# Kernel tuning notes

Hardware: AMD Instinct MI355X
Metric: run time of the kernel (lower is better)

The kernel has to match this reference:

```python
import jax, jax.numpy as jnp
import numpy as np
import math

# ---- HashGridEncoder constants (from init_kwargs) ----
L = 16            # levels
LOG2T = 19
T = 1 << LOG2T    # hash table size per level
F = 2             # features per entry
N_MIN = 16
N_MAX = 2048
N_PTS = 524288    # number of query points
BB_MIN = np.zeros(3, np.float32)
BB_MAX = np.ones(3, np.float32)
B = math.exp((math.log(N_MAX) - math.log(N_MIN)) / (L - 1))
RES = np.array([math.floor(N_MIN * B ** i) for i in range(L)], dtype=np.float32)  # per-level grid resolution
VERTS = np.array([[0,0,0],[0,0,1],[0,1,0],[0,1,1],[1,0,0],[1,0,1],[1,1,0],[1,1,1]], dtype=np.int32)  # 8 cube corners
PI = np.array([1, 2654435761, 805459861], dtype=np.uint32)  # spatial hash primes
MASK = np.uint32((1 << 19) - 1)  # hard-coded mask from source


def setup_inputs() -> dict:
    key = jax.random.key(0)
    k1, k2 = jax.random.split(key)
    xyz = jax.random.uniform(k1, (N_PTS, 3), dtype=jnp.float32)  # points inside bbox [0,1]^3
    # nn.init.uniform_(weight, -1e-4, 1e-4)
    tables = jax.random.uniform(k2, (L, T, F), minval=-1e-4, maxval=1e-4, dtype=jnp.float32)
    return {"xyz": xyz, "tables": tables}


def reference(xyz, tables):
    # cell size per level: (bb_max - bb_min) / resolution  -> [L,3]
    cell = (BB_MAX - BB_MIN)[None, :] / RES[:, None]
    # normalized grid coords for all levels at once: [L,N,3]
    u = (xyz[None, :, :] - BB_MIN) / cell[:, None, :]
    mi = jnp.floor(u).astype(jnp.int32)            # min corner index [L,N,3]
    d = u - mi.astype(jnp.float32)                 # trilinear fracs == (xyz - min_vertex)/cell, [L,N,3]
    # 8 corner integer coords: [L,N,8,3]; uint32 wrapping matches int64-mul + low-19-bit mask
    corners = (mi[:, :, None, :] + VERTS[None, None]).astype(jnp.uint32)
    h = (corners[..., 0] * PI[0]) ^ (corners[..., 1] * PI[1]) ^ (corners[..., 2] * PI[2])
    h = (h & MASK).astype(jnp.int32)               # hash indices [L,N,8], all < T
    # gather all levels in one flat lookup
    flat = tables.reshape(L * T, F)
    idx = h + (jnp.arange(L, dtype=jnp.int32) * T)[:, None, None]
    emb = flat[idx]                                # [L,N,8,F]
    # trilinear weights: prod over axes of d (corner bit 1) or 1-d (corner bit 0) -> [L,N,8]
    w = jnp.prod(jnp.where(VERTS[None, None].astype(bool), d[:, :, None, :], 1.0 - d[:, :, None, :]), axis=-1)
    c = jnp.einsum('lnv,lnvf->lnf', w, emb)        # interpolated features [L,N,F]
    # torch.cat(embedded, dim=-1): level-major concat -> [N, L*F]
    return jnp.moveaxis(c, 0, 1).reshape(xyz.shape[0], L * F)
```

## Files before the change

### kernel.cpp

```cpp
#include <hip/hip_runtime.h>
#include <cmath>

#define NLEVELS 16
#define HMASK   0x7FFFFu
#define NPTS    524288
#define NBUCKET 32768

typedef float v4f __attribute__((ext_vector_type(4)));
typedef float v2f __attribute__((ext_vector_type(2)));

struct LevelParams {
    float cell[NLEVELS];
};

__device__ __forceinline__ unsigned spread5(unsigned v) {
    return (v & 1u) | ((v & 2u) << 2) | ((v & 4u) << 4) |
           ((v & 8u) << 6) | ((v & 16u) << 8);
}

__device__ __forceinline__ unsigned morton_key(float x, float y, float z) {
    unsigned bx = min(31u, (unsigned)(x * 32.0f));
    unsigned by = min(31u, (unsigned)(y * 32.0f));
    unsigned bz = min(31u, (unsigned)(z * 32.0f));
    return spread5(bx) | (spread5(by) << 1) | (spread5(bz) << 2);
}

__device__ __forceinline__ void ngp_hash(
    float x, float y, float z, float cell, unsigned* __restrict__ h,
    float& dx, float& dy, float& dz)
{
    const float ux = x / cell;
    const float uy = y / cell;
    const float uz = z / cell;
    const float fx = floorf(ux);
    const float fy = floorf(uy);
    const float fz = floorf(uz);
    dx = ux - fx;
    dy = uy - fy;
    dz = uz - fz;

    const unsigned ix = (unsigned)(int)fx;
    const unsigned iy = (unsigned)(int)fy;
    const unsigned iz = (unsigned)(int)fz;

    const unsigned hx0 = ix;
    const unsigned hx1 = ix + 1u;
    const unsigned hy0 = iy * 2654435761u;
    const unsigned hy1 = (iy + 1u) * 2654435761u;
    const unsigned hz0 = iz * 805459861u;
    const unsigned hz1 = (iz + 1u) * 805459861u;

    h[0] = (hx0 ^ hy0 ^ hz0) & HMASK;
    h[1] = (hx0 ^ hy0 ^ hz1) & HMASK;
    h[2] = (hx0 ^ hy1 ^ hz0) & HMASK;
    h[3] = (hx0 ^ hy1 ^ hz1) & HMASK;
    h[4] = (hx1 ^ hy0 ^ hz0) & HMASK;
    h[5] = (hx1 ^ hy0 ^ hz1) & HMASK;
    h[6] = (hx1 ^ hy1 ^ hz0) & HMASK;
    h[7] = (hx1 ^ hy1 ^ hz1) & HMASK;
}

__device__ __forceinline__ void ngp_weights(
    float dx, float dy, float dz, float* __restrict__ w)
{
    const float wx0 = 1.0f - dx;
    const float wy0 = 1.0f - dy;
    const float wz0 = 1.0f - dz;
    const float p00 = wx0 * wy0;
    const float p01 = wx0 * dy;
    const float p10 = dx * wy0;
    const float p11 = dx * dy;
    w[0] = p00 * wz0;
    w[1] = p00 * dz;
    w[2] = p01 * wz0;
    w[3] = p01 * dz;
    w[4] = p10 * wz0;
    w[5] = p10 * dz;
    w[6] = p11 * wz0;
    w[7] = p11 * dz;
}

__device__ __forceinline__ v2f ngp_combine(
    const float* __restrict__ w, const v2f* __restrict__ e)
{
    float c0 = w[0] * e[0].x;
    float c1 = w[0] * e[0].y;
    #pragma unroll
    for (int c = 1; c < 8; ++c) {
        c0 += w[c] * e[c].x;
        c1 += w[c] * e[c].y;
    }
    v2f r = { c0, c1 };
    return r;
}

__global__ __launch_bounds__(256) void bucket_count(
    const float* __restrict__ xyz, unsigned* __restrict__ counts)
{
    const int n = blockIdx.x * 256 + threadIdx.x;
    const float x = xyz[3 * n + 0];
    const float y = xyz[3 * n + 1];
    const float z = xyz[3 * n + 2];
    atomicAdd(&counts[morton_key(x, y, z)], 1u);
}

__global__ __launch_bounds__(1024) void bucket_scan(
    const unsigned* __restrict__ counts, unsigned* __restrict__ cursor)
{
    __shared__ unsigned c[NBUCKET];
    __shared__ unsigned psum[1024];
    const unsigned t = threadIdx.x;

    #pragma unroll
    for (int i = 0; i < 32; ++i) {
        const unsigned idx = (unsigned)i * 1024u + t;
        c[idx ^ ((idx >> 5) & 31u)] = counts[idx];
    }
    __syncthreads();

    unsigned s = 0;
    #pragma unroll
    for (int i = 0; i < 32; ++i) {
        const unsigned idx = t * 32u + (unsigned)i;
        s += c[idx ^ ((idx >> 5) & 31u)];
    }
    psum[t] = s;
    __syncthreads();

    for (unsigned off = 1; off < 1024; off <<= 1) {
        unsigned v = 0;
        if (t >= off) v = psum[t - off];
        __syncthreads();
        if (t >= off) psum[t] += v;
        __syncthreads();
    }

    unsigned excl = psum[t] - s;
    #pragma unroll
    for (int i = 0; i < 32; ++i) {
        const unsigned idx = t * 32u + (unsigned)i;
        const unsigned sw  = idx ^ ((idx >> 5) & 31u);
        const unsigned v = c[sw];
        c[sw] = excl;
        excl += v;
    }
    __syncthreads();

    #pragma unroll
    for (int i = 0; i < 32; ++i) {
        const unsigned idx = (unsigned)i * 1024u + t;
        cursor[idx] = c[idx ^ ((idx >> 5) & 31u)];
    }
}

__global__ __launch_bounds__(256) void bucket_scatter(
    const float* __restrict__ xyz, unsigned* __restrict__ cursor,
    v4f* __restrict__ pts)
{
    const int n = blockIdx.x * 256 + threadIdx.x;
    const float x = xyz[3 * n + 0];
    const float y = xyz[3 * n + 1];
    const float z = xyz[3 * n + 2];
    const unsigned key = morton_key(x, y, z);
    const unsigned p = atomicAdd(&cursor[key], 1u);
    v4f v = { x, y, z, __uint_as_float((unsigned)n) };
    pts[p] = v;
}

__global__ __launch_bounds__(256) void ngp_phase1(
    const v4f* __restrict__ pts,
    const float* __restrict__ tables,
    v2f* __restrict__ ws,
    LevelParams lp)
{
    const unsigned b = blockIdx.x;
    const int level = (int)(b >> 11);
    const int chunk = (int)(b & 2047u);
    const int p = chunk * 256 + threadIdx.x;

    const v4f q = pts[p];

    const float cell = lp.cell[level];
    const v2f* __restrict__ tab = (const v2f*)tables + ((size_t)level << 19);

    unsigned h[8];
    float dx, dy, dz;
    ngp_hash(q.x, q.y, q.z, cell, h, dx, dy, dz);

    v2f e[8];
    if (level >= 7) {
        v2f e0, e1, e2, e3, e4, e5, e6, e7;
        const v2f* a0 = tab + h[0];
        const v2f* a1 = tab + h[1];
        const v2f* a2 = tab + h[2];
        const v2f* a3 = tab + h[3];
        const v2f* a4 = tab + h[4];
        const v2f* a5 = tab + h[5];
        const v2f* a6 = tab + h[6];
        const v2f* a7 = tab + h[7];
        asm volatile(
            "global_load_dwordx2 %0, %8, off sc0\n\t"
            "global_load_dwordx2 %1, %9, off sc0\n\t"
            "global_load_dwordx2 %2, %10, off sc0\n\t"
            "global_load_dwordx2 %3, %11, off sc0\n\t"
            "global_load_dwordx2 %4, %12, off sc0\n\t"
            "global_load_dwordx2 %5, %13, off sc0\n\t"
            "global_load_dwordx2 %6, %14, off sc0\n\t"
            "global_load_dwordx2 %7, %15, off sc0\n\t"
            "s_waitcnt vmcnt(0)"
            : "=&v"(e0), "=&v"(e1), "=&v"(e2), "=&v"(e3),
              "=&v"(e4), "=&v"(e5), "=&v"(e6), "=&v"(e7)
            : "v"(a0), "v"(a1), "v"(a2), "v"(a3),
              "v"(a4), "v"(a5), "v"(a6), "v"(a7));
        e[0] = e0; e[1] = e1; e[2] = e2; e[3] = e3;
        e[4] = e4; e[5] = e5; e[6] = e6; e[7] = e7;
    } else {
        #pragma unroll
        for (int c = 0; c < 8; ++c) e[c] = tab[h[c]];
    }

    float w[8];
    ngp_weights(dx, dy, dz, w);

    const v2f r = ngp_combine(w, e);

    __builtin_nontemporal_store(r, &ws[(size_t)level * NPTS + p]);
}

#define P2S 257

__global__ __launch_bounds__(256) void ngp_phase2(
    const v2f* __restrict__ ws,
    const v4f* __restrict__ pts,
    float* __restrict__ out)
{
    __shared__ v2f lds[NLEVELS * P2S];
    __shared__ unsigned nperm[256];
    const unsigned base = blockIdx.x * 256;
    const unsigned t = threadIdx.x;

    nperm[t] = __float_as_uint(pts[base + t].w);
    #pragma unroll
    for (int l = 0; l < NLEVELS; ++l)
        lds[l * P2S + t] =
            __builtin_nontemporal_load(&ws[(size_t)l * NPTS + base + t]);

    __syncthreads();

    #pragma unroll
    for (int it = 0; it < 8; ++it) {
        const unsigned j = it * 256 + t;
        const unsigned pl = j >> 3;
        const unsigned k = j & 7u;
        const v2f a = lds[(2u * k)      * P2S + pl];
        const v2f b = lds[(2u * k + 1u) * P2S + pl];
        v4f v = { a.x, a.y, b.x, b.y };
        __builtin_nontemporal_store(
            v, (v4f*)(out + (size_t)nperm[pl] * 32 + k * 4));
    }
}

__global__ __launch_bounds__(256) void ngp_encode(
    const float* __restrict__ xyz,
    const float* __restrict__ tables,
    float* __restrict__ out,
    LevelParams lp)
{
    const int n = blockIdx.x * 256 + threadIdx.x;
    const float x = xyz[3 * n + 0];
    const float y = xyz[3 * n + 1];
    const float z = xyz[3 * n + 2];

    float acc[2 * NLEVELS];
    const v2f* __restrict__ tab_base = (const v2f*)tables;

    #pragma unroll
    for (int l = 0; l < NLEVELS; ++l) {
        unsigned h[8];
        float dx, dy, dz;
        ngp_hash(x, y, z, lp.cell[l], h, dx, dy, dz);
        const v2f* __restrict__ tab = tab_base + ((size_t)l << 19);
        v2f e[8];
        #pragma unroll
        for (int c = 0; c < 8; ++c) e[c] = tab[h[c]];
        float w[8];
        ngp_weights(dx, dy, dz, w);
        const v2f r = ngp_combine(w, e);
        acc[2 * l + 0] = r.x;
        acc[2 * l + 1] = r.y;
    }

    v4f* o4 = (v4f*)(out + (size_t)n * 32);
    #pragma unroll
    for (int j = 0; j < 8; ++j) {
        v4f v = { acc[4 * j + 0], acc[4 * j + 1],
                  acc[4 * j + 2], acc[4 * j + 3] };
        o4[j] = v;
    }
}

extern "C" void kernel_launch(void* const* d_in, const int* in_sizes, int n_in,
                              void* d_out, int out_size, void* d_ws, size_t ws_size,
                              hipStream_t stream) {
    const float* xyz    = (const float*)d_in[0];
    const float* tables = (const float*)d_in[1];
    float* out          = (float*)d_out;

    LevelParams lp;
    const double B = std::exp((std::log(2048.0) - std::log(16.0)) / 15.0);
    for (int i = 0; i < NLEVELS; ++i) {
        const double r = std::floor(16.0 * std::pow(B, (double)i));
        lp.cell[i] = 1.0f / (float)r;
    }

    const size_t off_feat   = 0;
    const size_t off_pts    = off_feat + (size_t)NLEVELS * NPTS * sizeof(v2f);
    const size_t off_counts = off_pts + (size_t)NPTS * sizeof(v4f);
    const size_t off_cursor = off_counts + (size_t)NBUCKET * sizeof(unsigned);
    const size_t ws_needed  = off_cursor + (size_t)NBUCKET * sizeof(unsigned);

    if (ws_size >= ws_needed) {
        char* wsb = (char*)d_ws;
        v2f*      ws_feat = (v2f*)(wsb + off_feat);
        v4f*      pts     = (v4f*)(wsb + off_pts);
        unsigned* counts  = (unsigned*)(wsb + off_counts);
        unsigned* cursor  = (unsigned*)(wsb + off_cursor);

        hipMemsetAsync(counts, 0, NBUCKET * sizeof(unsigned), stream);
        hipLaunchKernelGGL(bucket_count, dim3(NPTS / 256), dim3(256), 0, stream,
                           xyz, counts);
        hipLaunchKernelGGL(bucket_scan, dim3(1), dim3(1024), 0, stream,
                           counts, cursor);
        hipLaunchKernelGGL(bucket_scatter, dim3(NPTS / 256), dim3(256), 0, stream,
                           xyz, cursor, pts);
        hipLaunchKernelGGL(ngp_phase1, dim3(NLEVELS * (NPTS / 256)), dim3(256), 0, stream,
                           pts, tables, ws_feat, lp);
        hipLaunchKernelGGL(ngp_phase2, dim3(NPTS / 256), dim3(256), 0, stream,
                           ws_feat, pts, out);
    } else {
        hipLaunchKernelGGL(ngp_encode, dim3(NPTS / 256), dim3(256), 0, stream,
                           xyz, tables, out, lp);
    }
}
```

Before: 351.1 us.

## Process two points per thread in phase1 and use wave-shuffle scan

Phase1 now handles two points per thread. It issues 16 table gathers before waiting, and computes the first point's result while the second point's loads are still in flight (vmcnt(8)). This raises memory-level parallelism per wave. The inline-asm gather path now covers levels from 5 instead of 7. The bucket scan replaces the 1024-wide LDS Hillis-Steele loop, which had many barriers, with a wave-level shuffle scan plus a 16-entry wave-sum pass. More registers per thread may lower occupancy, and the grid is halved.

Result: no change. 351.1 us (+0.0%).

```diff
diff --git a/kernel.cpp b/kernel.cpp
--- a/kernel.cpp
+++ b/kernel.cpp
@@ -108,8 +108,10 @@
     const unsigned* __restrict__ counts, unsigned* __restrict__ cursor)
 {
     __shared__ unsigned c[NBUCKET];
-    __shared__ unsigned psum[1024];
+    __shared__ unsigned wsum[16];
     const unsigned t = threadIdx.x;
+    const unsigned lane = t & 63u;
+    const unsigned wid = t >> 6;
 
     #pragma unroll
     for (int i = 0; i < 32; ++i) {
@@ -124,25 +126,29 @@
         const unsigned idx = t * 32u + (unsigned)i;
         s += c[idx ^ ((idx >> 5) & 31u)];
     }
-    psum[t] = s;
+
+    unsigned v = s;
+    #pragma unroll
+    for (unsigned off = 1; off < 64; off <<= 1) {
+        const unsigned u = __shfl_up(v, off);
+        if (lane >= off) v += u;
+    }
+    if (lane == 63u) wsum[wid] = v;
     __syncthreads();
 
-    for (unsigned off = 1; off < 1024; off <<= 1) {
-        unsigned v = 0;
-        if (t >= off) v = psum[t - off];
-        __syncthreads();
-        if (t >= off) psum[t] += v;
-        __syncthreads();
-    }
-
-    unsigned excl = psum[t] - s;
+    unsigned woff = 0;
+    #pragma unroll
+    for (unsigned w = 0; w < 16; ++w)
+        woff += (w < wid) ? wsum[w] : 0u;
+
+    unsigned excl = woff + (v - s);
     #pragma unroll
     for (int i = 0; i < 32; ++i) {
         const unsigned idx = t * 32u + (unsigned)i;
         const unsigned sw  = idx ^ ((idx >> 5) & 31u);
-        const unsigned v = c[sw];
+        const unsigned tmp = c[sw];
         c[sw] = excl;
-        excl += v;
+        excl += tmp;
     }
     __syncthreads();
 
@@ -174,30 +180,26 @@
     LevelParams lp)
 {
     const unsigned b = blockIdx.x;
-    const int level = (int)(b >> 11);
-    const int chunk = (int)(b & 2047u);
-    const int p = chunk * 256 + threadIdx.x;
-
-    const v4f q = pts[p];
+    const int level = (int)(b >> 10);
+    const int chunk = (int)(b & 1023u);
+    const int p0 = chunk * 512 + threadIdx.x;
+    const int p1 = p0 + 256;
+
+    const v4f qa = pts[p0];
+    const v4f qb = pts[p1];
 
     const float cell = lp.cell[level];
     const v2f* __restrict__ tab = (const v2f*)tables + ((size_t)level << 19);
 
-    unsigned h[8];
-    float dx, dy, dz;
-    ngp_hash(q.x, q.y, q.z, cell, h, dx, dy, dz);
-
-    v2f e[8];
-    if (level >= 7) {
-        v2f e0, e1, e2, e3, e4, e5, e6, e7;
-        const v2f* a0 = tab + h[0];
-        const v2f* a1 = tab + h[1];
-        const v2f* a2 = tab + h[2];
-        const v2f* a3 = tab + h[3];
-        const v2f* a4 = tab + h[4];
-        const v2f* a5 = tab + h[5];
-        const v2f* a6 = tab + h[6];
-        const v2f* a7 = tab + h[7];
+    unsigned ha[8], hb[8];
+    float dxa, dya, dza, dxb, dyb, dzb;
+    ngp_hash(qa.x, qa.y, qa.z, cell, ha, dxa, dya, dza);
+    ngp_hash(qb.x, qb.y, qb.z, cell, hb, dxb, dyb, dzb);
+
+    v2f ea[8], eb[8];
+    if (level >= 5) {
+        v2f a0, a1, a2, a3, a4, a5, a6, a7;
+        v2f b0, b1, b2, b3, b4, b5, b6, b7;
         asm volatile(
             "global_load_dwordx2 %0, %8, off sc0\n\t"
             "global_load_dwordx2 %1, %9, off sc0\n\t"
@@ -206,25 +208,63 @@
             "global_load_dwordx2 %4, %12, off sc0\n\t"
             "global_load_dwordx2 %5, %13, off sc0\n\t"
             "global_load_dwordx2 %6, %14, off sc0\n\t"
-            "global_load_dwordx2 %7, %15, off sc0\n\t"
+            "global_load_dwordx2 %7, %15, off sc0"
+            : "=&v"(a0), "=&v"(a1), "=&v"(a2), "=&v"(a3),
+              "=&v"(a4), "=&v"(a5), "=&v"(a6), "=&v"(a7)
+            : "v"(tab + ha[0]), "v"(tab + ha[1]), "v"(tab + ha[2]), "v"(tab + ha[3]),
+              "v"(tab + ha[4]), "v"(tab + ha[5]), "v"(tab + ha[6]), "v"(tab + ha[7]));
+        asm volatile(
+            "global_load_dwordx2 %0, %8, off sc0\n\t"
+            "global_load_dwordx2 %1, %9, off sc0\n\t"
+            "global_load_dwordx2 %2, %10, off sc0\n\t"
+            "global_load_dwordx2 %3, %11, off sc0\n\t"
+            "global_load_dwordx2 %4, %12, off sc0\n\t"
+            "global_load_dwordx2 %5, %13, off sc0\n\t"
+            "global_load_dwordx2 %6, %14, off sc0\n\t"
+            "global_load_dwordx2 %7, %15, off sc0"
+            : "=&v"(b0), "=&v"(b1), "=&v"(b2), "=&v"(b3),
+              "=&v"(b4), "=&v"(b5), "=&v"(b6), "=&v"(b7)
+            : "v"(tab + hb[0]), "v"(tab + hb[1]), "v"(tab + hb[2]), "v"(tab + hb[3]),
+              "v"(tab + hb[4]), "v"(tab + hb[5]), "v"(tab + hb[6]), "v"(tab + hb[7]));
+        asm volatile(
+            "s_waitcnt vmcnt(8)"
+            : "+v"(a0), "+v"(a1), "+v"(a2), "+v"(a3),
+              "+v"(a4), "+v"(a5), "+v"(a6), "+v"(a7));
+        ea[0] = a0; ea[1] = a1; ea[2] = a2; ea[3] = a3;
+        ea[4] = a4; ea[5] = a5; ea[6] = a6; ea[7] = a7;
+
+        float wa[8];
+        ngp_weights(dxa, dya, dza, wa);
+        const v2f ra = ngp_combine(wa, ea);
+
+        asm volatile(
             "s_waitcnt vmcnt(0)"
-            : "=&v"(e0), "=&v"(e1), "=&v"(e2), "=&v"(e3),
-              "=&v"(e4), "=&v"(e5), "=&v"(e6), "=&v"(e7)
-            : "v"(a0), "v"(a1), "v"(a2), "v"(a3),
-              "v"(a4), "v"(a5), "v"(a6), "v"(a7));
-        e[0] = e0; e[1] = e1; e[2] = e2; e[3] = e3;
-        e[4] = e4; e[5] = e5; e[6] = e6; e[7] = e7;
+            : "+v"(b0), "+v"(b1), "+v"(b2), "+v"(b3),
+              "+v"(b4), "+v"(b5), "+v"(b6), "+v"(b7));
+        eb[0] = b0; eb[1] = b1; eb[2] = b2; eb[3] = b3;
+        eb[4] = b4; eb[5] = b5; eb[6] = b6; eb[7] = b7;
+
+        float wb[8];
+        ngp_weights(dxb, dyb, dzb, wb);
+        const v2f rb = ngp_combine(wb, eb);
+
+        __builtin_nontemporal_store(ra, &ws[(size_t)level * NPTS + p0]);
+        __builtin_nontemporal_store(rb, &ws[(size_t)level * NPTS + p1]);
     } else {
         #pragma unroll
-        for (int c = 0; c < 8; ++c) e[c] = tab[h[c]];
-    }
-
-    float w[8];
-    ngp_weights(dx, dy, dz, w);
-
-    const v2f r = ngp_combine(w, e);
-
-    __builtin_nontemporal_store(r, &ws[(size_t)level * NPTS + p]);
+        for (int c = 0; c < 8; ++c) ea[c] = tab[ha[c]];
+        #pragma unroll
+        for (int c = 0; c < 8; ++c) eb[c] = tab[hb[c]];
+
+        float wa[8], wb[8];
+        ngp_weights(dxa, dya, dza, wa);
+        ngp_weights(dxb, dyb, dzb, wb);
+        const v2f ra = ngp_combine(wa, ea);
+        const v2f rb = ngp_combine(wb, eb);
+
+        __builtin_nontemporal_store(ra, &ws[(size_t)level * NPTS + p0]);
+        __builtin_nontemporal_store(rb, &ws[(size_t)level * NPTS + p1]);
+    }
 }
 
 #define P2S 257
@@ -333,7 +373,7 @@
                            counts, cursor);
         hipLaunchKernelGGL(bucket_scatter, dim3(NPTS / 256), dim3(256), 0, stream,
                            xyz, cursor, pts);
-        hipLaunchKernelGGL(ngp_phase1, dim3(NLEVELS * (NPTS / 256)), dim3(256), 0, stream,
+        hipLaunchKernelGGL(ngp_phase1, dim3(NLEVELS * (NPTS / 512)), dim3(256), 0, stream,
                            pts, tables, ws_feat, lp);
         hipLaunchKernelGGL(ngp_phase2, dim3(NPTS / 256), dim3(256), 0, stream,
                            ws_feat, pts, out);
```

## Fuse bucket sort into cooperative kernel and pair adjacent hash entries into 16-byte loads

Applied to the files above, without the earlier changes.

Replaces the memset, count, scan and scatter launches with one cooperative kernel that uses grid-wide syncs, removing several launches and the serial single-block scan. In phase1, levels from 5 upward use four dwordx4 loads when the x-corner index is even, because the x0 and x1 corner hashes then differ only in the low bit and share one aligned 16-byte slot. This cuts gather instructions for about half the points. The fallback bucket_scan also switches to a wave-shuffle scan. Risks include cooperative launch overhead and the cost of the grid syncs.

After: 793.0 us. 126% more time.

```diff
diff --git a/kernel.cpp b/kernel.cpp
--- a/kernel.cpp
+++ b/kernel.cpp
@@ -1,10 +1,14 @@
 #include <hip/hip_runtime.h>
+#include <hip/hip_cooperative_groups.h>
 #include <cmath>
+
+namespace cg = cooperative_groups;
 
 #define NLEVELS 16
 #define HMASK   0x7FFFFu
 #define NPTS    524288
 #define NBUCKET 32768
+#define SORTBLK 1024
 
 typedef float v4f __attribute__((ext_vector_type(4)));
 typedef float v2f __attribute__((ext_vector_type(2)));
@@ -27,7 +31,7 @@
 
 __device__ __forceinline__ void ngp_hash(
     float x, float y, float z, float cell, unsigned* __restrict__ h,
-    float& dx, float& dy, float& dz)
+    float& dx, float& dy, float& dz, unsigned& ix_out)
 {
     const float ux = x / cell;
     const float uy = y / cell;
@@ -42,6 +46,7 @@
     const unsigned ix = (unsigned)(int)fx;
     const unsigned iy = (unsigned)(int)fy;
     const unsigned iz = (unsigned)(int)fz;
+    ix_out = ix;
 
     const unsigned hx0 = ix;
     const unsigned hx1 = ix + 1u;
@@ -94,6 +99,95 @@
     return r;
 }
 
+__global__ __launch_bounds__(256, 4) void sort_coop(
+    const float* __restrict__ xyz,
+    v4f* __restrict__ pts,
+    unsigned* __restrict__ counts,
+    unsigned* __restrict__ cursor,
+    unsigned* __restrict__ bsum)
+{
+    cg::grid_group grid = cg::this_grid();
+    const unsigned b = blockIdx.x;
+    const unsigned t = threadIdx.x;
+    const unsigned lane = t & 63u;
+    const unsigned gtid = b * 256u + t;
+
+    if (gtid < NBUCKET) counts[gtid] = 0u;
+    grid.sync();
+
+    #pragma unroll
+    for (int k = 0; k < 2; ++k) {
+        const unsigned n = gtid + (unsigned)k * (NPTS / 2);
+        const float x = xyz[3 * n + 0];
+        const float y = xyz[3 * n + 1];
+        const float z = xyz[3 * n + 2];
+        atomicAdd(&counts[morton_key(x, y, z)], 1u);
+    }
+    grid.sync();
+
+    if (t < 64u) {
+        unsigned v = (t < 32u) ? counts[b * 32u + t] : 0u;
+        #pragma unroll
+        for (unsigned off = 1; off < 64; off <<= 1)
+            v += __shfl_xor(v, off);
+        if (t == 0u) bsum[b] = v;
+    }
+    grid.sync();
+
+    if (b == 0u) {
+        __shared__ unsigned wtot[4];
+        const unsigned wid = t >> 6;
+        const unsigned base = t * 4u;
+        const unsigned v0 = bsum[base + 0];
+        const unsigned v1 = bsum[base + 1];
+        const unsigned v2 = bsum[base + 2];
+        const unsigned v3 = bsum[base + 3];
+        const unsigned s = v0 + v1 + v2 + v3;
+        unsigned incl = s;
+        #pragma unroll
+        for (unsigned off = 1; off < 64; off <<= 1) {
+            const unsigned u = __shfl_up(incl, off);
+            if (lane >= off) incl += u;
+        }
+        if (lane == 63u) wtot[wid] = incl;
+        __syncthreads();
+        unsigned woff = 0;
+        #pragma unroll
+        for (unsigned w = 0; w < 4; ++w)
+            woff += (w < wid) ? wtot[w] : 0u;
+        const unsigned excl = woff + incl - s;
+        bsum[base + 0] = excl;
+        bsum[base + 1] = excl + v0;
+        bsum[base + 2] = excl + v0 + v1;
+        bsum[base + 3] = excl + v0 + v1 + v2;
+    }
+    grid.sync();
+
+    if (t < 64u) {
+        const unsigned v = (t < 32u) ? counts[b * 32u + t] : 0u;
+        unsigned incl = v;
+        #pragma unroll
+        for (unsigned off = 1; off < 64; off <<= 1) {
+            const unsigned u = __shfl_up(incl, off);
+            if (lane >= off) incl += u;
+        }
+        if (t < 32u) cursor[b * 32u + t] = bsum[b] + (incl - v);
+    }
+    grid.sync();
+
+    #pragma unroll
+    for (int k = 0; k < 2; ++k) {
+        const unsigned n = gtid + (unsigned)k * (NPTS / 2);
+        const float x = xyz[3 * n + 0];
+        const float y = xyz[3 * n + 1];
+        const float z = xyz[3 * n + 2];
+        const unsigned key = morton_key(x, y, z);
+        const unsigned p = atomicAdd(&cursor[key], 1u);
+        v4f v = { x, y, z, __uint_as_float(n) };
+        pts[p] = v;
+    }
+}
+
 __global__ __launch_bounds__(256) void bucket_count(
     const float* __restrict__ xyz, unsigned* __restrict__ counts)
 {
@@ -108,8 +202,10 @@
     const unsigned* __restrict__ counts, unsigned* __restrict__ cursor)
 {
     __shared__ unsigned c[NBUCKET];
-    __shared__ unsigned psum[1024];
+    __shared__ unsigned wsum[16];
     const unsigned t = threadIdx.x;
+    const unsigned lane = t & 63u;
+    const unsigned wid = t >> 6;
 
     #pragma unroll
     for (int i = 0; i < 32; ++i) {
@@ -124,25 +220,29 @@
         const unsigned idx = t * 32u + (unsigned)i;
         s += c[idx ^ ((idx >> 5) & 31u)];
     }
-    psum[t] = s;
+
+    unsigned v = s;
+    #pragma unroll
+    for (unsigned off = 1; off < 64; off <<= 1) {
+        const unsigned u = __shfl_up(v, off);
+        if (lane >= off) v += u;
+    }
+    if (lane == 63u) wsum[wid] = v;
     __syncthreads();
 
-    for (unsigned off = 1; off < 1024; off <<= 1) {
-        unsigned v = 0;
-        if (t >= off) v = psum[t - off];
-        __syncthreads();
-        if (t >= off) psum[t] += v;
-        __syncthreads();
-    }
-
-    unsigned excl = psum[t] - s;
+    unsigned woff = 0;
+    #pragma unroll
+    for (unsigned w = 0; w < 16; ++w)
+        woff += (w < wid) ? wsum[w] : 0u;
+
+    unsigned excl = woff + (v - s);
     #pragma unroll
     for (int i = 0; i < 32; ++i) {
         const unsigned idx = t * 32u + (unsigned)i;
         const unsigned sw  = idx ^ ((idx >> 5) & 31u);
-        const unsigned v = c[sw];
+        const unsigned tmp = c[sw];
         c[sw] = excl;
-        excl += v;
+        excl += tmp;
     }
     __syncthreads();
 
@@ -185,35 +285,61 @@
 
     unsigned h[8];
     float dx, dy, dz;
-    ngp_hash(q.x, q.y, q.z, cell, h, dx, dy, dz);
+    unsigned ix;
+    ngp_hash(q.x, q.y, q.z, cell, h, dx, dy, dz, ix);
 
     v2f e[8];
-    if (level >= 7) {
-        v2f e0, e1, e2, e3, e4, e5, e6, e7;
-        const v2f* a0 = tab + h[0];
-        const v2f* a1 = tab + h[1];
-        const v2f* a2 = tab + h[2];
-        const v2f* a3 = tab + h[3];
-        const v2f* a4 = tab + h[4];
-        const v2f* a5 = tab + h[5];
-        const v2f* a6 = tab + h[6];
-        const v2f* a7 = tab + h[7];
-        asm volatile(
-            "global_load_dwordx2 %0, %8, off sc0\n\t"
-            "global_load_dwordx2 %1, %9, off sc0\n\t"
-            "global_load_dwordx2 %2, %10, off sc0\n\t"
-            "global_load_dwordx2 %3, %11, off sc0\n\t"
-            "global_load_dwordx2 %4, %12, off sc0\n\t"
-            "global_load_dwordx2 %5, %13, off sc0\n\t"
-            "global_load_dwordx2 %6, %14, off sc0\n\t"
-            "global_load_dwordx2 %7, %15, off sc0\n\t"
-            "s_waitcnt vmcnt(0)"
-            : "=&v"(e0), "=&v"(e1), "=&v"(e2), "=&v"(e3),
-              "=&v"(e4), "=&v"(e5), "=&v"(e6), "=&v"(e7)
-            : "v"(a0), "v"(a1), "v"(a2), "v"(a3),
-              "v"(a4), "v"(a5), "v"(a6), "v"(a7));
-        e[0] = e0; e[1] = e1; e[2] = e2; e[3] = e3;
-        e[4] = e4; e[5] = e5; e[6] = e6; e[7] = e7;
+    if (level >= 5) {
+        if (!(ix & 1u)) {
+            v4f p0, p1, p2, p3;
+            const v4f* a0 = (const v4f*)(tab + (h[0] & ~1u));
+            const v4f* a1 = (const v4f*)(tab + (h[1] & ~1u));
+            const v4f* a2 = (const v4f*)(tab + (h[2] & ~1u));
+            const v4f* a3 = (const v4f*)(tab + (h[3] & ~1u));
+            asm volatile(
+                "global_load_dwordx4 %0, %4, off sc0\n\t"
+                "global_load_dwordx4 %1, %5, off sc0\n\t"
+                "global_load_dwordx4 %2, %6, off sc0\n\t"
+                "global_load_dwordx4 %3, %7, off sc0"
+                : "=&v"(p0), "=&v"(p1), "=&v"(p2), "=&v"(p3)
+                : "v"(a0), "v"(a1), "v"(a2), "v"(a3));
+            asm volatile(
+                "s_waitcnt vmcnt(0)"
+                : "+v"(p0), "+v"(p1), "+v"(p2), "+v"(p3));
+            const bool o0 = (h[0] & 1u) != 0u;
+            const bool o1 = (h[1] & 1u) != 0u;
+            const bool o2 = (h[2] & 1u) != 0u;
+            const bool o3 = (h[3] & 1u) != 0u;
+            e[0].x = o0 ? p0.z : p0.x;  e[0].y = o0 ? p0.w : p0.y;
+            e[4].x = o0 ? p0.x : p0.z;  e[4].y = o0 ? p0.y : p0.w;
+            e[1].x = o1 ? p1.z : p1.x;  e[1].y = o1 ? p1.w : p1.y;
+            e[5].x = o1 ? p1.x : p1.z;  e[5].y = o1 ? p1.y : p1.w;
+            e[2].x = o2 ? p2.z : p2.x;  e[2].y = o2 ? p2.w : p2.y;
+            e[6].x = o2 ? p2.x : p2.z;  e[6].y = o2 ? p2.y : p2.w;
+            e[3].x = o3 ? p3.z : p3.x;  e[3].y = o3 ? p3.w : p3.y;
+            e[7].x = o3 ? p3.x : p3.z;  e[7].y = o3 ? p3.y : p3.w;
+        } else {
+            v2f e0, e1, e2, e3, e4, e5, e6, e7;
+            asm volatile(
+                "global_load_dwordx2 %0, %8, off sc0\n\t"
+                "global_load_dwordx2 %1, %9, off sc0\n\t"
+                "global_load_dwordx2 %2, %10, off sc0\n\t"
+                "global_load_dwordx2 %3, %11, off sc0\n\t"
+                "global_load_dwordx2 %4, %12, off sc0\n\t"
+                "global_load_dwordx2 %5, %13, off sc0\n\t"
+                "global_load_dwordx2 %6, %14, off sc0\n\t"
+                "global_load_dwordx2 %7, %15, off sc0"
+                : "=&v"(e0), "=&v"(e1), "=&v"(e2), "=&v"(e3),
+                  "=&v"(e4), "=&v"(e5), "=&v"(e6), "=&v"(e7)
+                : "v"(tab + h[0]), "v"(tab + h[1]), "v"(tab + h[2]), "v"(tab + h[3]),
+                  "v"(tab + h[4]), "v"(tab + h[5]), "v"(tab + h[6]), "v"(tab + h[7]));
+            asm volatile(
+                "s_waitcnt vmcnt(0)"
+                : "+v"(e0), "+v"(e1), "+v"(e2), "+v"(e3),
+                  "+v"(e4), "+v"(e5), "+v"(e6), "+v"(e7));
+            e[0] = e0; e[1] = e1; e[2] = e2; e[3] = e3;
+            e[4] = e4; e[5] = e5; e[6] = e6; e[7] = e7;
+        }
     } else {
         #pragma unroll
         for (int c = 0; c < 8; ++c) e[c] = tab[h[c]];
@@ -278,7 +404,8 @@
     for (int l = 0; l < NLEVELS; ++l) {
         unsigned h[8];
         float dx, dy, dz;
-        ngp_hash(x, y, z, lp.cell[l], h, dx, dy, dz);
+        unsigned ix;
+        ngp_hash(x, y, z, lp.cell[l], h, dx, dy, dz, ix);
         const v2f* __restrict__ tab = tab_base + ((size_t)l << 19);
         v2f e[8];
         #pragma unroll
@@ -317,7 +444,8 @@
     const size_t off_pts    = off_feat + (size_t)NLEVELS * NPTS * sizeof(v2f);
     const size_t off_counts = off_pts + (size_t)NPTS * sizeof(v4f);
     const size_t off_cursor = off_counts + (size_t)NBUCKET * sizeof(unsigned);
-    const size_t ws_needed  = off_cursor + (size_t)NBUCKET * sizeof(unsigned);
+    const size_t off_bsum   = off_cursor + (size_t)NBUCKET * sizeof(unsigned);
+    const size_t ws_needed  = off_bsum + (size_t)SORTBLK * sizeof(unsigned);
 
     if (ws_size >= ws_needed) {
         char* wsb = (char*)d_ws;
@@ -325,14 +453,21 @@
         v4f*      pts     = (v4f*)(wsb + off_pts);
         unsigned* counts  = (unsigned*)(wsb + off_counts);
         unsigned* cursor  = (unsigned*)(wsb + off_cursor);
-
-        hipMemsetAsync(counts, 0, NBUCKET * sizeof(unsigned), stream);
-        hipLaunchKernelGGL(bucket_count, dim3(NPTS / 256), dim3(256), 0, stream,
-                           xyz, counts);
-        hipLaunchKernelGGL(bucket_scan, dim3(1), dim3(1024), 0, stream,
-                           counts, cursor);
-        hipLaunchKernelGGL(bucket_scatter, dim3(NPTS / 256), dim3(256), 0, stream,
-                           xyz, cursor, pts);
+        unsigned* bsum    = (unsigned*)(wsb + off_bsum);
+
+        void* args[] = { (void*)&xyz, (void*)&pts, (void*)&counts,
+                         (void*)&cursor, (void*)&bsum };
+        const hipError_t cerr = hipLaunchCooperativeKernel(
+            (const void*)sort_coop, dim3(SORTBLK), dim3(256), args, 0, stream);
+        if (cerr != hipSuccess) {
+            hipMemsetAsync(counts, 0, NBUCKET * sizeof(unsigned), stream);
+            hipLaunchKernelGGL(bucket_count, dim3(NPTS / 256), dim3(256), 0, stream,
+                               xyz, counts);
+            hipLaunchKernelGGL(bucket_scan, dim3(1), dim3(1024), 0, stream,
+                               counts, cursor);
+            hipLaunchKernelGGL(bucket_scatter, dim3(NPTS / 256), dim3(256), 0, stream,
+                               xyz, cursor, pts);
+        }
         hipLaunchKernelGGL(ngp_phase1, dim3(NLEVELS * (NPTS / 256)), dim3(256), 0, stream,
                            pts, tables, ws_feat, lp);
         hipLaunchKernelGGL(ngp_phase2, dim3(NPTS / 256), dim3(256), 0, stream,
```

## Pair x-adjacent hash corners into 16-byte loads when ix is even

Applied to the files above, without the earlier changes.

When the x cell index is even, corners c and c+4 differ only in the low hash bit, so both entries sit in the same aligned 16-byte pair. The phase-1 kernel then issues four dwordx4 gathers instead of eight dwordx2 gathers and picks the halves by parity. The asm-load threshold moves from level 7 to level 5, and the wait is split into a separate asm. The bucket scan also replaces its barrier-heavy shared-memory Hillis-Steele scan with wavefront shuffles plus a 16-entry per-wave sum. The paired path adds divergence between threads with even and odd ix.

Result: faster. 331.7 us (-5.5%).

```diff
diff --git a/kernel.cpp b/kernel.cpp
--- a/kernel.cpp
+++ b/kernel.cpp
@@ -27,7 +27,7 @@
 
 __device__ __forceinline__ void ngp_hash(
     float x, float y, float z, float cell, unsigned* __restrict__ h,
-    float& dx, float& dy, float& dz)
+    float& dx, float& dy, float& dz, unsigned& ix_out)
 {
     const float ux = x / cell;
     const float uy = y / cell;
@@ -42,6 +42,7 @@
     const unsigned ix = (unsigned)(int)fx;
     const unsigned iy = (unsigned)(int)fy;
     const unsigned iz = (unsigned)(int)fz;
+    ix_out = ix;
 
     const unsigned hx0 = ix;
     const unsigned hx1 = ix + 1u;
@@ -108,8 +109,10 @@
     const unsigned* __restrict__ counts, unsigned* __restrict__ cursor)
 {
     __shared__ unsigned c[NBUCKET];
-    __shared__ unsigned psum[1024];
+    __shared__ unsigned wsum[16];
     const unsigned t = threadIdx.x;
+    const unsigned lane = t & 63u;
+    const unsigned wid = t >> 6;
 
     #pragma unroll
     for (int i = 0; i < 32; ++i) {
@@ -124,25 +127,29 @@
         const unsigned idx = t * 32u + (unsigned)i;
         s += c[idx ^ ((idx >> 5) & 31u)];
     }
-    psum[t] = s;
+
+    unsigned v = s;
+    #pragma unroll
+    for (unsigned off = 1; off < 64; off <<= 1) {
+        const unsigned u = __shfl_up(v, off);
+        if (lane >= off) v += u;
+    }
+    if (lane == 63u) wsum[wid] = v;
     __syncthreads();
 
-    for (unsigned off = 1; off < 1024; off <<= 1) {
-        unsigned v = 0;
-        if (t >= off) v = psum[t - off];
-        __syncthreads();
-        if (t >= off) psum[t] += v;
-        __syncthreads();
-    }
-
-    unsigned excl = psum[t] - s;
+    unsigned woff = 0;
+    #pragma unroll
+    for (unsigned w = 0; w < 16; ++w)
+        woff += (w < wid) ? wsum[w] : 0u;
+
+    unsigned excl = woff + (v - s);
     #pragma unroll
     for (int i = 0; i < 32; ++i) {
         const unsigned idx = t * 32u + (unsigned)i;
         const unsigned sw  = idx ^ ((idx >> 5) & 31u);
-        const unsigned v = c[sw];
+        const unsigned tmp = c[sw];
         c[sw] = excl;
-        excl += v;
+        excl += tmp;
     }
     __syncthreads();
 
@@ -185,38 +192,74 @@
 
     unsigned h[8];
     float dx, dy, dz;
-    ngp_hash(q.x, q.y, q.z, cell, h, dx, dy, dz);
+    unsigned ix;
+    ngp_hash(q.x, q.y, q.z, cell, h, dx, dy, dz, ix);
 
     v2f e[8];
-    if (level >= 7) {
-        v2f e0, e1, e2, e3, e4, e5, e6, e7;
-        const v2f* a0 = tab + h[0];
-        const v2f* a1 = tab + h[1];
-        const v2f* a2 = tab + h[2];
-        const v2f* a3 = tab + h[3];
-        const v2f* a4 = tab + h[4];
-        const v2f* a5 = tab + h[5];
-        const v2f* a6 = tab + h[6];
-        const v2f* a7 = tab + h[7];
-        asm volatile(
-            "global_load_dwordx2 %0, %8, off sc0\n\t"
-            "global_load_dwordx2 %1, %9, off sc0\n\t"
-            "global_load_dwordx2 %2, %10, off sc0\n\t"
-            "global_load_dwordx2 %3, %11, off sc0\n\t"
-            "global_load_dwordx2 %4, %12, off sc0\n\t"
-            "global_load_dwordx2 %5, %13, off sc0\n\t"
-            "global_load_dwordx2 %6, %14, off sc0\n\t"
-            "global_load_dwordx2 %7, %15, off sc0\n\t"
-            "s_waitcnt vmcnt(0)"
-            : "=&v"(e0), "=&v"(e1), "=&v"(e2), "=&v"(e3),
-              "=&v"(e4), "=&v"(e5), "=&v"(e6), "=&v"(e7)
-            : "v"(a0), "v"(a1), "v"(a2), "v"(a3),
-              "v"(a4), "v"(a5), "v"(a6), "v"(a7));
-        e[0] = e0; e[1] = e1; e[2] = e2; e[3] = e3;
-        e[4] = e4; e[5] = e5; e[6] = e6; e[7] = e7;
+    if (!(ix & 1u)) {
+        if (level >= 5) {
+            v4f p0, p1, p2, p3;
+            const v4f* a0 = (const v4f*)(tab + (h[0] & ~1u));
+            const v4f* a1 = (const v4f*)(tab + (h[1] & ~1u));
+            const v4f* a2 = (const v4f*)(tab + (h[2] & ~1u));
+            const v4f* a3 = (const v4f*)(tab + (h[3] & ~1u));
+            asm volatile(
+                "global_load_dwordx4 %0, %4, off sc0\n\t"
+                "global_load_dwordx4 %1, %5, off sc0\n\t"
+                "global_load_dwordx4 %2, %6, off sc0\n\t"
+                "global_load_dwordx4 %3, %7, off sc0"
+                : "=&v"(p0), "=&v"(p1), "=&v"(p2), "=&v"(p3)
+                : "v"(a0), "v"(a1), "v"(a2), "v"(a3));
+            asm volatile(
+                "s_waitcnt vmcnt(0)"
+                : "+v"(p0), "+v"(p1), "+v"(p2), "+v"(p3));
+            const bool o0 = (h[0] & 1u) != 0u;
+            const bool o1 = (h[1] & 1u) != 0u;
+            const bool o2 = (h[2] & 1u) != 0u;
+            const bool o3 = (h[3] & 1u) != 0u;
+            e[0].x = o0 ? p0.z : p0.x;  e[0].y = o0 ? p0.w : p0.y;
+            e[4].x = o0 ? p0.x : p0.z;  e[4].y = o0 ? p0.y : p0.w;
+            e[1].x = o1 ? p1.z : p1.x;  e[1].y = o1 ? p1.w : p1.y;
+            e[5].x = o1 ? p1.x : p1.z;  e[5].y = o1 ? p1.y : p1.w;
+            e[2].x = o2 ? p2.z : p2.x;  e[2].y = o2 ? p2.w : p2.y;
+            e[6].x = o2 ? p2.x : p2.z;  e[6].y = o2 ? p2.y : p2.w;
+            e[3].x = o3 ? p3.z : p3.x;  e[3].y = o3 ? p3.w : p3.y;
+            e[7].x = o3 ? p3.x : p3.z;  e[7].y = o3 ? p3.y : p3.w;
+        } else {
+            #pragma unroll
+            for (int c = 0; c < 4; ++c) {
+                const v4f pv = *(const v4f*)(tab + (h[c] & ~1u));
+                const bool o = (h[c] & 1u) != 0u;
+                e[c].x     = o ? pv.z : pv.x;  e[c].y     = o ? pv.w : pv.y;
+                e[c + 4].x = o ? pv.x : pv.z;  e[c + 4].y = o ? pv.y : pv.w;
+            }
+        }
     } else {
-        #pragma unroll
-        for (int c = 0; c < 8; ++c) e[c] = tab[h[c]];
+        if (level >= 5) {
+            v2f e0, e1, e2, e3, e4, e5, e6, e7;
+            asm volatile(
+                "global_load_dwordx2 %0, %8, off sc0\n\t"
+                "global_load_dwordx2 %1, %9, off sc0\n\t"
+                "global_load_dwordx2 %2, %10, off sc0\n\t"
+                "global_load_dwordx2 %3, %11, off sc0\n\t"
+                "global_load_dwordx2 %4, %12, off sc0\n\t"
+                "global_load_dwordx2 %5, %13, off sc0\n\t"
+                "global_load_dwordx2 %6, %14, off sc0\n\t"
+                "global_load_dwordx2 %7, %15, off sc0"
+                : "=&v"(e0), "=&v"(e1), "=&v"(e2), "=&v"(e3),
+                  "=&v"(e4), "=&v"(e5), "=&v"(e6), "=&v"(e7)
+                : "v"(tab + h[0]), "v"(tab + h[1]), "v"(tab + h[2]), "v"(tab + h[3]),
+                  "v"(tab + h[4]), "v"(tab + h[5]), "v"(tab + h[6]), "v"(tab + h[7]));
+            asm volatile(
+                "s_waitcnt vmcnt(0)"
+                : "+v"(e0), "+v"(e1), "+v"(e2), "+v"(e3),
+                  "+v"(e4), "+v"(e5), "+v"(e6), "+v"(e7));
+            e[0] = e0; e[1] = e1; e[2] = e2; e[3] = e3;
+            e[4] = e4; e[5] = e5; e[6] = e6; e[7] = e7;
+        } else {
+            #pragma unroll
+            for (int c = 0; c < 8; ++c) e[c] = tab[h[c]];
+        }
     }
 
     float w[8];
@@ -278,7 +321,8 @@
     for (int l = 0; l < NLEVELS; ++l) {
         unsigned h[8];
         float dx, dy, dz;
-        ngp_hash(x, y, z, lp.cell[l], h, dx, dy, dz);
+        unsigned ix;
+        ngp_hash(x, y, z, lp.cell[l], h, dx, dy, dz, ix);
         const v2f* __restrict__ tab = tab_base + ((size_t)l << 19);
         v2f e[8];
         #pragma unroll
```
